# Performance work log

Measured on AMD Instinct MI355X. Metric: run time of the kernel, lower is better.

## Reference

```python
import jax, jax.numpy as jnp
import numpy as np

EPS = 1e-5

def mish(x):
    return x * jnp.tanh(jax.nn.softplus(x))

def masked_bn(x, masks, w, b, rm, rv):
    # eval-mode masked batchnorm: normalize with running stats, zero masked-out positions
    out = w * ((x - rm) / jnp.sqrt(rv + EPS)) + b
    return jnp.where(masks, out, jnp.zeros((), dtype=out.dtype))

def channel_shuffle(x):
    B, C, L = x.shape
    cpg = C // 2
    y = jnp.pad(x, ((0, 0), (1, 1), (0, 0)))          # [B, C+2, L]
    y = y.reshape(B, 2, cpg + 1, L)
    y = jnp.transpose(y, (0, 2, 1, 3)).reshape(B, -1, L)
    return y[:, 1:-1, :]

def setup_inputs() -> dict:
    key = jax.random.key(0)
    ks = jax.random.split(key, 8)
    B, C, L = 32, 512, 4096
    br = C // 2
    x = jax.random.normal(ks[0], (B, C, L), dtype=jnp.float32)
    masks = jax.random.randint(ks[1], (B, 1, L), 0, 2) > 0
    s = 1.0 / np.sqrt(br)
    w1 = jax.random.normal(ks[2], (br, br, 1), dtype=jnp.float32) * s
    w2 = jax.random.normal(ks[3], (br, 1, 3), dtype=jnp.float32) * (1.0 / np.sqrt(3.0))
    w3 = jax.random.normal(ks[4], (br, br, 1), dtype=jnp.float32) * s
    def bn_params(k):
        k1, k2 = jax.random.split(k)
        return (jnp.ones((br, 1), jnp.float32), jnp.zeros((br, 1), jnp.float32),
                jax.random.normal(k1, (br, 1), jnp.float32) * 0.1,
                jnp.abs(jax.random.normal(k2, (br, 1), jnp.float32)) * 0.1 + 0.9)
    bn1 = bn_params(ks[5]); bn2 = bn_params(ks[6]); bn3 = bn_params(ks[7])
    return {"x": x, "masks": masks, "w1": w1, "w2": w2, "w3": w3,
            "bn1_w": bn1[0], "bn1_b": bn1[1], "bn1_rm": bn1[2], "bn1_rv": bn1[3],
            "bn2_w": bn2[0], "bn2_b": bn2[1], "bn2_rm": bn2[2], "bn2_rv": bn2[3],
            "bn3_w": bn3[0], "bn3_b": bn3[1], "bn3_rm": bn3[2], "bn3_rv": bn3[3]}

def reference(x, masks, w1, w2, w3,
              bn1_w, bn1_b, bn1_rm, bn1_rv,
              bn2_w, bn2_b, bn2_rm, bn2_rv,
              bn3_w, bn3_b, bn3_rm, bn3_rv):
    C = x.shape[1]
    x1, x2 = x[:, :C // 2, :], x[:, C // 2:, :]
    br = C // 2
    # conv_1: 1x1 pointwise -> GEMM
    b2 = jnp.einsum('oi,bil->bol', w1[:, :, 0], x2)
    b2 = mish(b2)
    b2 = masked_bn(b2, masks, bn1_w, bn1_b, bn1_rm, bn1_rv)
    # conv_2: depthwise k=3, pad=1
    b2 = jax.lax.conv_general_dilated(
        b2, w2, window_strides=(1,), padding=((1, 1),),
        dimension_numbers=('NCH', 'OIH', 'NCH'), feature_group_count=br)
    b2 = masked_bn(b2, masks, bn2_w, bn2_b, bn2_rm, bn2_rv)
    # conv_3: 1x1 pointwise
    b2 = jnp.einsum('oi,bil->bol', w3[:, :, 0], b2)
    b2 = mish(b2)
    b2 = masked_bn(b2, masks, bn3_w, bn3_b, bn3_rm, bn3_rv)
    # dropout: identity in eval mode
    out = jnp.concatenate([x1, b2], axis=1)
    return channel_shuffle(out)
```

## Files before the change

### kernel.cpp

```cpp
#include <hip/hip_runtime.h>
#include <cmath>

#define BATCH 32
#define CIN   512
#define BR    256
#define LEN   4096
#define TL    32
#define ROWS  34
#define RS    264
#define NBLK  128

typedef __attribute__((ext_vector_type(8))) short bf16x8;
typedef __attribute__((ext_vector_type(4))) float f32x4;

#define MFMA_BF16(a,b,c) __builtin_amdgcn_mfma_f32_16x16x32_bf16((a),(b),(c),0,0,0)

__device__ __forceinline__ float bf2f(unsigned short h){
  union { unsigned int u; float f; } c; c.u = ((unsigned int)h) << 16; return c.f;
}
__device__ __forceinline__ unsigned short f2bf(float f){
  union { float f; unsigned int u; } c; c.f = f;
  unsigned int r = c.u + 0x7fffu + ((c.u >> 16) & 1u);
  return (unsigned short)(r >> 16);
}
__device__ __forceinline__ float mish_f(float v){
  float p = __expf(fminf(v, 40.0f));
  float u = p * (p + 2.0f);
  return v * (u / (u + 2.0f));
}
__device__ __forceinline__ void unpack8(const uint4 v, float* f){
  f[0] = bf2f((unsigned short)(v.x & 0xffffu)); f[1] = bf2f((unsigned short)(v.x >> 16));
  f[2] = bf2f((unsigned short)(v.y & 0xffffu)); f[3] = bf2f((unsigned short)(v.y >> 16));
  f[4] = bf2f((unsigned short)(v.z & 0xffffu)); f[5] = bf2f((unsigned short)(v.z >> 16));
  f[6] = bf2f((unsigned short)(v.w & 0xffffu)); f[7] = bf2f((unsigned short)(v.w >> 16));
}

__global__ void prep_kernel(const float* __restrict__ w1, const float* __restrict__ w2,
                            const float* __restrict__ w3,
                            const float* __restrict__ b1w, const float* __restrict__ b1b,
                            const float* __restrict__ b1rm, const float* __restrict__ b1rv,
                            const float* __restrict__ b2w, const float* __restrict__ b2b,
                            const float* __restrict__ b2rm, const float* __restrict__ b2rv,
                            const float* __restrict__ b3w, const float* __restrict__ b3b,
                            const float* __restrict__ b3rm, const float* __restrict__ b3rv,
                            unsigned short* __restrict__ w1bf, unsigned short* __restrict__ w3bf,
                            float* __restrict__ folds)
{
  const int g = blockIdx.x * 256 + threadIdx.x;
  w1bf[g] = f2bf(w1[g]);
  w3bf[g] = f2bf(w3[g]);
  if (blockIdx.x == 0) {
    const int c = threadIdx.x;
    float a1 = b1w[c] / sqrtf(b1rv[c] + 1e-5f);
    folds[c]        = a1; folds[256 + c]  = b1b[c] - b1rm[c] * a1;
    float a2 = b2w[c] / sqrtf(b2rv[c] + 1e-5f);
    folds[512 + c]  = a2; folds[768 + c]  = b2b[c] - b2rm[c] * a2;
    float a3 = b3w[c] / sqrtf(b3rv[c] + 1e-5f);
    folds[1024 + c] = a3; folds[1280 + c] = b3b[c] - b3rm[c] * a3;
    folds[1536 + c] = w2[c * 3 + 0];
    folds[1792 + c] = w2[c * 3 + 1];
    folds[2048 + c] = w2[c * 3 + 2];
  }
}

__global__ __launch_bounds__(256)
void copy_x1_kernel(const float* __restrict__ xg, float* __restrict__ outg)
{
  const int k  = blockIdx.x;
  const int bb = k >> 8;
  const int c  = k & 255;
  const float4* __restrict__ src = (const float4*)(xg  + (size_t)(bb * CIN + c)         * LEN);
  float4*       __restrict__ dst = (float4*)      (outg + (size_t)(bb * CIN + 2 * c + 1) * LEN);
  const int t = threadIdx.x;
  const float4 v0 = src[t];
  const float4 v1 = src[t + 256];
  const float4 v2 = src[t + 512];
  const float4 v3 = src[t + 768];
  dst[t]       = v0;
  dst[t + 256] = v1;
  dst[t + 512] = v2;
  dst[t + 768] = v3;
}

__global__ __launch_bounds__(256, 4)
void fused_main(const float* __restrict__ xg,
                const int*   __restrict__ maskg,
                const unsigned short* __restrict__ w1bf,
                const unsigned short* __restrict__ w3bf,
                const float* __restrict__ fa1, const float* __restrict__ fb1,
                const float* __restrict__ fa2, const float* __restrict__ fb2,
                const float* __restrict__ fa3, const float* __restrict__ fb3,
                const float* __restrict__ w2p,
                float*       __restrict__ outg)
{
  __shared__ __align__(16) unsigned short ls_x2[ROWS * RS];
  __shared__ __align__(16) unsigned short ls_t1[ROWS * RS];
  __shared__ int ls_mk[48];

  const int tid = threadIdx.x;
  const int bx  = blockIdx.x;
  const int b   = blockIdx.y;
  const int l0  = bx * TL;

  float4 stg[10];
  #pragma unroll
  for (int it = 0; it < 10; ++it) {
    const int q   = tid + 256 * it;
    const int c   = q / 10;
    const int j   = q - 10 * c;
    const int lg  = l0 - 4 + 4 * j;
    const int lgc = min(max(lg, 0), LEN - 4);
    stg[it] = *(const float4*)(xg + (size_t)(b * CIN + BR + c) * LEN + lgc);
  }

  if (bx == 0 || bx == NBLK - 1) {
    uint4* z = (uint4*)ls_x2;
    const uint4 zz = make_uint4(0, 0, 0, 0);
    for (int i = tid; i < (ROWS * RS) / 8; i += 256) z[i] = zz;
  }
  if (tid < 48) {
    const int l = l0 - 1 + tid;
    ls_mk[tid] = (tid < ROWS && l >= 0 && l < LEN) ? maskg[b * LEN + l] : 0;
  }
  __syncthreads();

  #pragma unroll
  for (int it = 0; it < 10; ++it) {
    const int q   = tid + 256 * it;
    const int c   = q / 10;
    const int j   = q - 10 * c;
    const int lg  = l0 - 4 + 4 * j;
    const int lgc = min(max(lg, 0), LEN - 4);
    const float vv[4] = {stg[it].x, stg[it].y, stg[it].z, stg[it].w};
    #pragma unroll
    for (int jj = 0; jj < 4; ++jj) {
      const int p = (lgc + jj) - (l0 - 1);
      if (p >= 0 && p < ROWS) ls_x2[p * RS + c] = f2bf(vv[jj]);
    }
  }
  __syncthreads();

  const int lane = tid & 63;
  const int wid  = tid >> 6;
  const int xl   = lane & 15;
  const int qd   = lane >> 4;

  {
    int mk1[3];
    #pragma unroll
    for (int j = 0; j < 3; ++j)
      mk1[j] = ls_mk[16 * j + xl];
    #pragma unroll
    for (int mi = 0; mi < 4; ++mi) {
      const int ob = (wid * 4 + mi) * 16;
      bf16x8 af[8];
      #pragma unroll
      for (int k = 0; k < 8; ++k)
        af[k] = *(const bf16x8*)&w1bf[(size_t)(ob + xl) * 256 + k * 32 + qd * 8];
      const f32x4 av = *(const f32x4*)&fa1[ob + 4 * qd];
      const f32x4 bv = *(const f32x4*)&fb1[ob + 4 * qd];
      #pragma unroll
      for (int j = 0; j < 3; ++j) {
        const int p  = 16 * j + xl;
        const int rp = min(p, ROWS - 1);
        bf16x8 bfr[8];
        #pragma unroll
        for (int k = 0; k < 8; ++k)
          bfr[k] = *(const bf16x8*)&ls_x2[rp * RS + k * 32 + qd * 8];
        f32x4 acc = {0.f, 0.f, 0.f, 0.f};
        #pragma unroll
        for (int k = 0; k < 8; ++k) acc = MFMA_BF16(af[k], bfr[k], acc);
        unsigned short us[4];
        #pragma unroll
        for (int r = 0; r < 4; ++r) {
          float v = mish_f(acc[r]);
          v = av[r] * v + bv[r];
          if (!mk1[j]) v = 0.0f;
          us[r] = f2bf(v);
        }
        if (p < ROWS) {
          const unsigned int lo = (unsigned int)us[0] | ((unsigned int)us[1] << 16);
          const unsigned int hi = (unsigned int)us[2] | ((unsigned int)us[3] << 16);
          *(uint2*)&ls_t1[p * RS + ob + 4 * qd] = make_uint2(lo, hi);
        }
      }
    }
  }
  __syncthreads();

  {
    const int c0    = (tid & 31) * 8;
    const int qbase = tid >> 5;
    const f32x4 k0a = *(const f32x4*)&w2p[      c0], k0b = *(const f32x4*)&w2p[      c0 + 4];
    const f32x4 k1a = *(const f32x4*)&w2p[256 + c0], k1b = *(const f32x4*)&w2p[256 + c0 + 4];
    const f32x4 k2a = *(const f32x4*)&w2p[512 + c0], k2b = *(const f32x4*)&w2p[512 + c0 + 4];
    const f32x4 a2a = *(const f32x4*)&fa2[c0],       a2b = *(const f32x4*)&fa2[c0 + 4];
    const f32x4 b2a = *(const f32x4*)&fb2[c0],       b2b = *(const f32x4*)&fb2[c0 + 4];
    #pragma unroll
    for (int it = 0; it < 4; ++it) {
      const int qo = qbase + 8 * it;
      const int mk = ls_mk[1 + qo];
      const uint4 ra = *(const uint4*)&ls_t1[(qo    ) * RS + c0];
      const uint4 rb = *(const uint4*)&ls_t1[(qo + 1) * RS + c0];
      const uint4 rc = *(const uint4*)&ls_t1[(qo + 2) * RS + c0];
      float ta[8], tb[8], tc[8];
      unpack8(ra, ta); unpack8(rb, tb); unpack8(rc, tc);
      unsigned short us[8];
      #pragma unroll
      for (int i = 0; i < 4; ++i) {
        float y  = a2a[i] * (k0a[i] * ta[i]     + k1a[i] * tb[i]     + k2a[i] * tc[i]    ) + b2a[i];
        float y2 = a2b[i] * (k0b[i] * ta[4 + i] + k1b[i] * tb[4 + i] + k2b[i] * tc[4 + i]) + b2b[i];
        if (!mk) { y = 0.0f; y2 = 0.0f; }
        us[i]     = f2bf(y);
        us[4 + i] = f2bf(y2);
      }
      uint4 wv;
      wv.x = (unsigned int)us[0] | ((unsigned int)us[1] << 16);
      wv.y = (unsigned int)us[2] | ((unsigned int)us[3] << 16);
      wv.z = (unsigned int)us[4] | ((unsigned int)us[5] << 16);
      wv.w = (unsigned int)us[6] | ((unsigned int)us[7] << 16);
      *(uint4*)&ls_x2[qo * RS + c0] = wv;
    }
  }
  __syncthreads();

  {
    int mks[2][4];
    #pragma unroll
    for (int j = 0; j < 2; ++j)
      #pragma unroll
      for (int r = 0; r < 4; ++r)
        mks[j][r] = ls_mk[1 + 16 * j + 4 * qd + r];
    #pragma unroll
    for (int mi = 0; mi < 4; ++mi) {
      const int ob = (wid * 4 + mi) * 16;
      bf16x8 af[8];
      #pragma unroll
      for (int k = 0; k < 8; ++k)
        af[k] = *(const bf16x8*)&w3bf[(size_t)(ob + xl) * 256 + k * 32 + qd * 8];
      const float a3v = fa3[ob + xl];
      const float b3v = fb3[ob + xl];
      #pragma unroll
      for (int j = 0; j < 2; ++j) {
        bf16x8 ta2[8];
        #pragma unroll
        for (int k = 0; k < 8; ++k)
          ta2[k] = *(const bf16x8*)&ls_x2[(16 * j + xl) * RS + k * 32 + qd * 8];
        f32x4 acc = {0.f, 0.f, 0.f, 0.f};
        #pragma unroll
        for (int k = 0; k < 8; ++k) acc = MFMA_BF16(ta2[k], af[k], acc);
        float4 ov;
        float* op = &ov.x;
        #pragma unroll
        for (int r = 0; r < 4; ++r) {
          float v = mish_f(acc[r]);
          v = a3v * v + b3v;
          if (!mks[j][r]) v = 0.0f;
          op[r] = v;
        }
        *(float4*)&outg[(size_t)(b * CIN + 2 * (ob + xl)) * LEN + l0 + 16 * j + 4 * qd] = ov;
      }
    }
  }
}

extern "C" void kernel_launch(void* const* d_in, const int* in_sizes, int n_in,
                              void* d_out, int out_size, void* d_ws, size_t ws_size,
                              hipStream_t stream) {
  (void)in_sizes; (void)n_in; (void)out_size; (void)ws_size;
  const float* xg    = (const float*)d_in[0];
  const int*   maskg = (const int*)d_in[1];
  const float* w1    = (const float*)d_in[2];
  const float* w2    = (const float*)d_in[3];
  const float* w3    = (const float*)d_in[4];
  const float* b1w   = (const float*)d_in[5];
  const float* b1b   = (const float*)d_in[6];
  const float* b1rm  = (const float*)d_in[7];
  const float* b1rv  = (const float*)d_in[8];
  const float* b2w   = (const float*)d_in[9];
  const float* b2b   = (const float*)d_in[10];
  const float* b2rm  = (const float*)d_in[11];
  const float* b2rv  = (const float*)d_in[12];
  const float* b3w   = (const float*)d_in[13];
  const float* b3b   = (const float*)d_in[14];
  const float* b3rm  = (const float*)d_in[15];
  const float* b3rv  = (const float*)d_in[16];
  float* outp = (float*)d_out;

  unsigned short* w1bf = (unsigned short*)d_ws;
  unsigned short* w3bf = (unsigned short*)((char*)d_ws + 131072);
  float*          folds = (float*)((char*)d_ws + 262144);

  hipLaunchKernelGGL(prep_kernel, dim3(256), dim3(256), 0, stream,
                     w1, w2, w3,
                     b1w, b1b, b1rm, b1rv, b2w, b2b, b2rm, b2rv, b3w, b3b, b3rm, b3rv,
                     w1bf, w3bf, folds);

  hipLaunchKernelGGL(copy_x1_kernel, dim3(BATCH * BR), dim3(256, 1, 1), 0, stream,
                     xg, outp);

  hipLaunchKernelGGL(fused_main, dim3(NBLK, BATCH, 1), dim3(256, 1, 1), 0, stream,
                     xg, maskg, w1bf, w3bf,
                     folds, folds + 256,
                     folds + 512, folds + 768,
                     folds + 1024, folds + 1280,
                     folds + 1536,
                     outp);
}
```

Measured before the change: 595.9 us.

## Fuse x1 passthrough copy into main kernel and simplify staging loads

Removes the separate copy kernel and folds the x1 channel copy into fused_main. Each block loads and stores a slice of x1 interleaved with its MFMA phases, so that passthrough traffic overlaps compute. It also changes the x2 staging so each thread loads one whole channel row, folds the BN2 scale into the depthwise weights, swaps the divide in mish for a reciprocal, and uses the library bf16 conversion. The cost is extra register pressure for the held float4 values. Staging also now writes one channel per thread into shared memory with strided access, which may cause bank conflicts.

```diff
diff --git a/kernel.cpp b/kernel.cpp
--- a/kernel.cpp
+++ b/kernel.cpp
@@ -1,4 +1,5 @@
 #include <hip/hip_runtime.h>
+#include <hip/hip_bf16.h>
 #include <cmath>
 
 #define BATCH 32
@@ -18,15 +19,16 @@
 __device__ __forceinline__ float bf2f(unsigned short h){
   union { unsigned int u; float f; } c; c.u = ((unsigned int)h) << 16; return c.f;
 }
-__device__ __forceinline__ unsigned short f2bf(float f){
-  union { float f; unsigned int u; } c; c.f = f;
-  unsigned int r = c.u + 0x7fffu + ((c.u >> 16) & 1u);
-  return (unsigned short)(r >> 16);
+__device__ __forceinline__ unsigned short cvt1(float f){
+  union { __hip_bfloat16 h; unsigned short u; } c; c.h = __float2bfloat16(f); return c.u;
+}
+__device__ __forceinline__ unsigned int pack2(float a, float b){
+  return (unsigned int)cvt1(a) | ((unsigned int)cvt1(b) << 16);
 }
 __device__ __forceinline__ float mish_f(float v){
   float p = __expf(fminf(v, 40.0f));
   float u = p * (p + 2.0f);
-  return v * (u / (u + 2.0f));
+  return v * u * __builtin_amdgcn_rcpf(u + 2.0f);
 }
 __device__ __forceinline__ void unpack8(const uint4 v, float* f){
   f[0] = bf2f((unsigned short)(v.x & 0xffffu)); f[1] = bf2f((unsigned short)(v.x >> 16));
@@ -47,39 +49,20 @@
                             float* __restrict__ folds)
 {
   const int g = blockIdx.x * 256 + threadIdx.x;
-  w1bf[g] = f2bf(w1[g]);
-  w3bf[g] = f2bf(w3[g]);
+  w1bf[g] = cvt1(w1[g]);
+  w3bf[g] = cvt1(w3[g]);
   if (blockIdx.x == 0) {
     const int c = threadIdx.x;
     float a1 = b1w[c] / sqrtf(b1rv[c] + 1e-5f);
     folds[c]        = a1; folds[256 + c]  = b1b[c] - b1rm[c] * a1;
     float a2 = b2w[c] / sqrtf(b2rv[c] + 1e-5f);
-    folds[512 + c]  = a2; folds[768 + c]  = b2b[c] - b2rm[c] * a2;
+    folds[768 + c]  = b2b[c] - b2rm[c] * a2;
     float a3 = b3w[c] / sqrtf(b3rv[c] + 1e-5f);
     folds[1024 + c] = a3; folds[1280 + c] = b3b[c] - b3rm[c] * a3;
-    folds[1536 + c] = w2[c * 3 + 0];
-    folds[1792 + c] = w2[c * 3 + 1];
-    folds[2048 + c] = w2[c * 3 + 2];
-  }
-}
-
-__global__ __launch_bounds__(256)
-void copy_x1_kernel(const float* __restrict__ xg, float* __restrict__ outg)
-{
-  const int k  = blockIdx.x;
-  const int bb = k >> 8;
-  const int c  = k & 255;
-  const float4* __restrict__ src = (const float4*)(xg  + (size_t)(bb * CIN + c)         * LEN);
-  float4*       __restrict__ dst = (float4*)      (outg + (size_t)(bb * CIN + 2 * c + 1) * LEN);
-  const int t = threadIdx.x;
-  const float4 v0 = src[t];
-  const float4 v1 = src[t + 256];
-  const float4 v2 = src[t + 512];
-  const float4 v3 = src[t + 768];
-  dst[t]       = v0;
-  dst[t + 256] = v1;
-  dst[t + 512] = v2;
-  dst[t + 768] = v3;
+    folds[1536 + c] = a2 * w2[c * 3 + 0];
+    folds[1792 + c] = a2 * w2[c * 3 + 1];
+    folds[2048 + c] = a2 * w2[c * 3 + 2];
+  }
 }
 
 __global__ __launch_bounds__(256, 4)
@@ -88,7 +71,7 @@
                 const unsigned short* __restrict__ w1bf,
                 const unsigned short* __restrict__ w3bf,
                 const float* __restrict__ fa1, const float* __restrict__ fb1,
-                const float* __restrict__ fa2, const float* __restrict__ fb2,
+                const float* __restrict__ fb2,
                 const float* __restrict__ fa3, const float* __restrict__ fb3,
                 const float* __restrict__ w2p,
                 float*       __restrict__ outg)
@@ -102,40 +85,49 @@
   const int b   = blockIdx.y;
   const int l0  = bx * TL;
 
+  const size_t xstr = (size_t)NBLK * BATCH * 256;
+  const size_t i0   = ((size_t)b * NBLK + bx) * 256 + tid;
+
+  float4 x1v[4];
+  #pragma unroll
+  for (int k = 0; k < 4; ++k) {
+    const size_t idx = i0 + (size_t)k * xstr;
+    const int l  = (int)((idx & 1023) * 4);
+    const int c  = (int)((idx >> 10) & 255);
+    const int bb = (int)(idx >> 18);
+    x1v[k] = *(const float4*)(xg + (size_t)(bb * CIN + c) * LEN + l);
+  }
+
   float4 stg[10];
-  #pragma unroll
-  for (int it = 0; it < 10; ++it) {
-    const int q   = tid + 256 * it;
-    const int c   = q / 10;
-    const int j   = q - 10 * c;
-    const int lg  = l0 - 4 + 4 * j;
-    const int lgc = min(max(lg, 0), LEN - 4);
-    stg[it] = *(const float4*)(xg + (size_t)(b * CIN + BR + c) * LEN + lgc);
+  {
+    const float* xrow = xg + (size_t)(b * CIN + BR + tid) * LEN;
+    #pragma unroll
+    for (int j = 0; j < 10; ++j) {
+      const int lgc = min(max(l0 - 4 + 4 * j, 0), LEN - 4);
+      stg[j] = *(const float4*)(xrow + lgc);
+    }
+  }
+
+  if (tid < 48) {
+    const int l = l0 - 1 + tid;
+    ls_mk[tid] = (tid < 48 && tid < ROWS && l >= 0 && l < LEN) ? maskg[b * LEN + l] : 0;
   }
 
   if (bx == 0 || bx == NBLK - 1) {
     uint4* z = (uint4*)ls_x2;
     const uint4 zz = make_uint4(0, 0, 0, 0);
     for (int i = tid; i < (ROWS * RS) / 8; i += 256) z[i] = zz;
-  }
-  if (tid < 48) {
-    const int l = l0 - 1 + tid;
-    ls_mk[tid] = (tid < ROWS && l >= 0 && l < LEN) ? maskg[b * LEN + l] : 0;
-  }
-  __syncthreads();
+    __syncthreads();
+  }
 
   #pragma unroll
-  for (int it = 0; it < 10; ++it) {
-    const int q   = tid + 256 * it;
-    const int c   = q / 10;
-    const int j   = q - 10 * c;
-    const int lg  = l0 - 4 + 4 * j;
-    const int lgc = min(max(lg, 0), LEN - 4);
-    const float vv[4] = {stg[it].x, stg[it].y, stg[it].z, stg[it].w};
+  for (int j = 0; j < 10; ++j) {
+    const int lgc = min(max(l0 - 4 + 4 * j, 0), LEN - 4);
+    const float* sp = (const float*)&stg[j];
     #pragma unroll
     for (int jj = 0; jj < 4; ++jj) {
       const int p = (lgc + jj) - (l0 - 1);
-      if (p >= 0 && p < ROWS) ls_x2[p * RS + c] = f2bf(vv[jj]);
+      if (p >= 0 && p < ROWS) ls_x2[p * RS + tid] = cvt1(sp[jj]);
     }
   }
   __syncthreads();
@@ -145,7 +137,26 @@
   const int xl   = lane & 15;
   const int qd   = lane >> 4;
 
+  float4 x1w[4];
+
   {
+    #pragma unroll
+    for (int k = 0; k < 4; ++k) {
+      const size_t idx = i0 + (size_t)k * xstr;
+      const int l  = (int)((idx & 1023) * 4);
+      const int c  = (int)((idx >> 10) & 255);
+      const int bb = (int)(idx >> 18);
+      *(float4*)(outg + (size_t)(bb * CIN + 2 * c + 1) * LEN + l) = x1v[k];
+    }
+    #pragma unroll
+    for (int k = 4; k < 8; ++k) {
+      const size_t idx = i0 + (size_t)k * xstr;
+      const int l  = (int)((idx & 1023) * 4);
+      const int c  = (int)((idx >> 10) & 255);
+      const int bb = (int)(idx >> 18);
+      x1w[k - 4] = *(const float4*)(xg + (size_t)(bb * CIN + c) * LEN + l);
+    }
+
     int mk1[3];
     #pragma unroll
     for (int j = 0; j < 3; ++j)
@@ -170,18 +181,17 @@
         f32x4 acc = {0.f, 0.f, 0.f, 0.f};
         #pragma unroll
         for (int k = 0; k < 8; ++k) acc = MFMA_BF16(af[k], bfr[k], acc);
-        unsigned short us[4];
+        float y[4];
         #pragma unroll
         for (int r = 0; r < 4; ++r) {
           float v = mish_f(acc[r]);
           v = av[r] * v + bv[r];
           if (!mk1[j]) v = 0.0f;
-          us[r] = f2bf(v);
+          y[r] = v;
         }
         if (p < ROWS) {
-          const unsigned int lo = (unsigned int)us[0] | ((unsigned int)us[1] << 16);
-          const unsigned int hi = (unsigned int)us[2] | ((unsigned int)us[3] << 16);
-          *(uint2*)&ls_t1[p * RS + ob + 4 * qd] = make_uint2(lo, hi);
+          *(uint2*)&ls_t1[p * RS + ob + 4 * qd] =
+              make_uint2(pack2(y[0], y[1]), pack2(y[2], y[3]));
         }
       }
     }
@@ -189,12 +199,20 @@
   __syncthreads();
 
   {
+    #pragma unroll
+    for (int k = 0; k < 4; ++k) {
+      const size_t idx = i0 + (size_t)(k + 4) * xstr;
+      const int l  = (int)((idx & 1023) * 4);
+      const int c  = (int)((idx >> 10) & 255);
+      const int bb = (int)(idx >> 18);
+      *(float4*)(outg + (size_t)(bb * CIN + 2 * c + 1) * LEN + l) = x1w[k];
+    }
+
     const int c0    = (tid & 31) * 8;
     const int qbase = tid >> 5;
     const f32x4 k0a = *(const f32x4*)&w2p[      c0], k0b = *(const f32x4*)&w2p[      c0 + 4];
     const f32x4 k1a = *(const f32x4*)&w2p[256 + c0], k1b = *(const f32x4*)&w2p[256 + c0 + 4];
     const f32x4 k2a = *(const f32x4*)&w2p[512 + c0], k2b = *(const f32x4*)&w2p[512 + c0 + 4];
-    const f32x4 a2a = *(const f32x4*)&fa2[c0],       a2b = *(const f32x4*)&fa2[c0 + 4];
     const f32x4 b2a = *(const f32x4*)&fb2[c0],       b2b = *(const f32x4*)&fb2[c0 + 4];
     #pragma unroll
     for (int it = 0; it < 4; ++it) {
@@ -205,20 +223,19 @@
       const uint4 rc = *(const uint4*)&ls_t1[(qo + 2) * RS + c0];
       float ta[8], tb[8], tc[8];
       unpack8(ra, ta); unpack8(rb, tb); unpack8(rc, tc);
-      unsigned short us[8];
+      float y[8];
       #pragma unroll
       for (int i = 0; i < 4; ++i) {
-        float y  = a2a[i] * (k0a[i] * ta[i]     + k1a[i] * tb[i]     + k2a[i] * tc[i]    ) + b2a[i];
-        float y2 = a2b[i] * (k0b[i] * ta[4 + i] + k1b[i] * tb[4 + i] + k2b[i] * tc[4 + i]) + b2b[i];
-        if (!mk) { y = 0.0f; y2 = 0.0f; }
-        us[i]     = f2bf(y);
-        us[4 + i] = f2bf(y2);
+        y[i]     = fmaf(k0a[i], ta[i],     fmaf(k1a[i], tb[i],     fmaf(k2a[i], tc[i],     b2a[i])));
+        y[4 + i] = fmaf(k0b[i], ta[4 + i], fmaf(k1b[i], tb[4 + i], fmaf(k2b[i], tc[4 + i], b2b[i])));
       }
+      #pragma unroll
+      for (int i = 0; i < 8; ++i) if (!mk) y[i] = 0.0f;
       uint4 wv;
-      wv.x = (unsigned int)us[0] | ((unsigned int)us[1] << 16);
-      wv.y = (unsigned int)us[2] | ((unsigned int)us[3] << 16);
-      wv.z = (unsigned int)us[4] | ((unsigned int)us[5] << 16);
-      wv.w = (unsigned int)us[6] | ((unsigned int)us[7] << 16);
+      wv.x = pack2(y[0], y[1]);
+      wv.y = pack2(y[2], y[3]);
+      wv.z = pack2(y[4], y[5]);
+      wv.w = pack2(y[6], y[7]);
       *(uint4*)&ls_x2[qo * RS + c0] = wv;
     }
   }
@@ -296,13 +313,10 @@
                      b1w, b1b, b1rm, b1rv, b2w, b2b, b2rm, b2rv, b3w, b3b, b3rm, b3rv,
                      w1bf, w3bf, folds);
 
-  hipLaunchKernelGGL(copy_x1_kernel, dim3(BATCH * BR), dim3(256, 1, 1), 0, stream,
-                     xg, outp);
-
   hipLaunchKernelGGL(fused_main, dim3(NBLK, BATCH, 1), dim3(256, 1, 1), 0, stream,
                      xg, maskg, w1bf, w3bf,
                      folds, folds + 256,
-                     folds + 512, folds + 768,
+                     folds + 768,
                      folds + 1024, folds + 1280,
                      folds + 1536,
                      outp);
```

Result: slower. 616.4 us (+3.4%).
